# Kernel tuning notes

Measured on AMD Instinct MI355X. Metric: run time of the kernel, lower is better.

Reference implementation:

```python
import jax, jax.numpy as jnp
import numpy as np

MEM_DIM = 1024
N_CHILD = 16384

def _linear_params(key, out_dim, in_dim):
    kw, kb = jax.random.split(key)
    bound = 1.0 / np.sqrt(in_dim)
    W = jax.random.uniform(kw, (out_dim, in_dim), jnp.float32, -bound, bound)
    b = jax.random.uniform(kb, (out_dim,), jnp.float32, -bound, bound)
    return W, b

def setup_inputs() -> dict:
    key = jax.random.key(0)
    ks = jax.random.split(key, 7)
    child_c = jax.random.normal(ks[0], (N_CHILD, MEM_DIM), jnp.float32)
    child_h = jax.random.normal(ks[1], (N_CHILD, MEM_DIM), jnp.float32)
    child_h_sum = jax.random.normal(ks[2], (MEM_DIM,), jnp.float32)
    W_ih, b_ih = _linear_params(ks[3], MEM_DIM, MEM_DIM)
    W_fh, b_fh = _linear_params(ks[4], MEM_DIM, MEM_DIM)
    W_uh, b_uh = _linear_params(ks[5], MEM_DIM, MEM_DIM)
    W_oh, b_oh = _linear_params(ks[6], MEM_DIM, MEM_DIM)
    return {
        "child_c": child_c, "child_h": child_h, "child_h_sum": child_h_sum,
        "W_ih": W_ih, "b_ih": b_ih, "W_fh": W_fh, "b_fh": b_fh,
        "W_uh": W_uh, "b_uh": b_uh, "W_oh": W_oh, "b_oh": b_oh,
    }

def reference(child_c, child_h, child_h_sum,
              W_ih, b_ih, W_fh, b_fh, W_uh, b_uh, W_oh, b_oh):
    # Gate projections on the summed child hidden state: [mem_dim]
    i = jax.nn.sigmoid(child_h_sum @ W_ih.T + b_ih)
    o = jax.nn.sigmoid(child_h_sum @ W_oh.T + b_oh)
    u = jnp.tanh(child_h_sum @ W_uh.T + b_uh)
    # Per-child forget gates, batched (replaces the Python loop): [N, mem_dim]
    f = jax.nn.sigmoid(child_h @ W_fh.T + b_fh)
    fc = f * child_c                     # [N, mem_dim]
    c = i * u + jnp.sum(fc, axis=0)      # [mem_dim]
    h = o * jnp.tanh(c)                  # [mem_dim]
    return (c, h)
```

## Files before the change

kernel.cpp:

```cpp
#include <hip/hip_runtime.h>
#include <hip/hip_bf16.h>
#include <math.h>

#define MEM_DIM 1024
#define N_CHILD 16384

#define BM 128
#define BN 64
#define BK 64
#define KITERS (MEM_DIM / BK)

typedef __bf16 bf16_t;
typedef __bf16 bf16x4 __attribute__((ext_vector_type(4)));
typedef __bf16 bf16x8 __attribute__((ext_vector_type(8)));
typedef float f32x4 __attribute__((ext_vector_type(4)));

__device__ __forceinline__ void async_load16(const bf16_t* g, bf16_t* l) {
    __builtin_amdgcn_global_load_lds(
        (const __attribute__((address_space(1))) unsigned int*)g,
        (__attribute__((address_space(3))) unsigned int*)l,
        16, 0, 0);
}

__global__ __launch_bounds__(256) void cvt_bf16_kernel(const float* __restrict__ srcA, int n8A,
                                                       const float* __restrict__ srcB, int n8B,
                                                       bf16_t* __restrict__ dst) {
    int t = blockIdx.x * 256 + threadIdx.x;
    if (t < n8A + n8B) {
        const float* s = (t < n8A) ? (srcA + (size_t)t * 8)
                                   : (srcB + (size_t)(t - n8A) * 8);
        float4 a = *(const float4*)s;
        float4 b = *(const float4*)(s + 4);
        bf16x8 o = { (bf16_t)a.x, (bf16_t)a.y, (bf16_t)a.z, (bf16_t)a.w,
                     (bf16_t)b.x, (bf16_t)b.y, (bf16_t)b.z, (bf16_t)b.w };
        *(bf16x8*)(dst + (size_t)t * 8) = o;
    }
}

__global__ void gates_kernel(const float* __restrict__ hsum,
                             const float* __restrict__ W_ih, const float* __restrict__ b_ih,
                             const float* __restrict__ W_uh, const float* __restrict__ b_uh,
                             const float* __restrict__ W_oh, const float* __restrict__ b_oh,
                             float* __restrict__ acc_c, float* __restrict__ o_ws) {
    const int j = blockIdx.x;
    const int tid = threadIdx.x;
    const float* wi = W_ih + (size_t)j * MEM_DIM;
    const float* wu = W_uh + (size_t)j * MEM_DIM;
    const float* wo = W_oh + (size_t)j * MEM_DIM;
    float si = 0.f, su = 0.f, so = 0.f;
    for (int k = tid; k < MEM_DIM; k += 256) {
        float hv = hsum[k];
        si += wi[k] * hv;
        su += wu[k] * hv;
        so += wo[k] * hv;
    }
    for (int off = 32; off > 0; off >>= 1) {
        si += __shfl_down(si, off, 64);
        su += __shfl_down(su, off, 64);
        so += __shfl_down(so, off, 64);
    }
    __shared__ float red[3][4];
    const int wave = tid >> 6, lane = tid & 63;
    if (lane == 0) { red[0][wave] = si; red[1][wave] = su; red[2][wave] = so; }
    __syncthreads();
    if (tid == 0) {
        float ti = red[0][0] + red[0][1] + red[0][2] + red[0][3] + b_ih[j];
        float tu = red[1][0] + red[1][1] + red[1][2] + red[1][3] + b_uh[j];
        float to = red[2][0] + red[2][1] + red[2][2] + red[2][3] + b_oh[j];
        float iv = 1.f / (1.f + expf(-ti));
        float uv = tanhf(tu);
        float ov = 1.f / (1.f + expf(-to));
        acc_c[j] = iv * uv;
        o_ws[j]  = ov;
    }
}

__global__ __launch_bounds__(256, 4) void fused_gemm_bf16(
        const bf16_t* __restrict__ hbf, const bf16_t* __restrict__ wbf,
        const float* __restrict__ child_c, const float* __restrict__ b_fh,
        float* __restrict__ acc_c) {
    __shared__ __align__(1024) bf16_t sA[BM * BK];
    __shared__ __align__(1024) bf16_t sB[BN * BK];
    __shared__ float sred[BN];

    const int tid  = threadIdx.x;
    const int lane = tid & 63;
    const int wave = tid >> 6;
    const int wr = wave >> 1;
    const int wc = wave & 1;
    const int q  = lane >> 4;
    const int cl = lane & 15;

    const int b   = blockIdx.x;
    const int xcd = b & 7;
    const int l   = b >> 3;
    const int jt  = l & 15;
    const int ntl = l >> 4;
    const int j0  = jt * BN;
    const int n0  = (xcd * 16 + ntl) * BM;

    const int rl = lane >> 3;
    const int p  = lane & 7;
    const int cf = (p ^ rl) * 8;
    const bf16_t* gA[4];
    bf16_t* lA[4];
#pragma unroll
    for (int i = 0; i < 4; i++) {
        const int r = wave * 32 + i * 8 + rl;
        gA[i] = hbf + (size_t)(n0 + r) * MEM_DIM + cf;
        lA[i] = &sA[(wave * 32 + i * 8) * BK];
    }
    const bf16_t* gB[2];
    bf16_t* lB[2];
#pragma unroll
    for (int i = 0; i < 2; i++) {
        const int r = wave * 16 + i * 8 + rl;
        gB[i] = wbf + (size_t)(j0 + r) * MEM_DIM + cf;
        lB[i] = &sB[(wave * 16 + i * 8) * BK];
    }

    f32x4 acc[4][2];
#pragma unroll
    for (int a = 0; a < 4; a++)
#pragma unroll
        for (int c = 0; c < 2; c++) acc[a][c] = (f32x4)0.0f;

    for (int k = 0; k < KITERS; ++k) {
#pragma unroll
        for (int i = 0; i < 4; i++) { async_load16(gA[i], lA[i]); gA[i] += BK; }
#pragma unroll
        for (int i = 0; i < 2; i++) { async_load16(gB[i], lB[i]); gB[i] += BK; }
        __syncthreads();

#pragma unroll
        for (int h = 0; h < 2; h++) {
            bf16x8 af[4], bfr[2];
#pragma unroll
            for (int mt = 0; mt < 4; mt++) {
                const int ra = wr * 64 + mt * 16 + cl;
                af[mt] = *(const bf16x8*)(&sA[ra * BK + (((4 * h + q) ^ (cl & 7)) * 8)]);
            }
#pragma unroll
            for (int nt = 0; nt < 2; nt++) {
                const int rb = wc * 32 + nt * 16 + cl;
                bfr[nt] = *(const bf16x8*)(&sB[rb * BK + (((4 * h + q) ^ (cl & 7)) * 8)]);
            }
#pragma unroll
            for (int mt = 0; mt < 4; mt++)
#pragma unroll
                for (int nt = 0; nt < 2; nt++)
                    acc[mt][nt] = __builtin_amdgcn_mfma_f32_16x16x32_bf16(
                        af[mt], bfr[nt], acc[mt][nt], 0, 0, 0);
        }
        __syncthreads();
    }

    if (tid < BN) sred[tid] = 0.0f;
    __syncthreads();

    float colsum[2] = {0.f, 0.f};
#pragma unroll
    for (int nt = 0; nt < 2; nt++) {
        const int col = j0 + wc * 32 + nt * 16 + cl;
        const float bias = b_fh[col];
#pragma unroll
        for (int mt = 0; mt < 4; mt++) {
#pragma unroll
            for (int r = 0; r < 4; r++) {
                const int row = n0 + wr * 64 + mt * 16 + q * 4 + r;
                float s = acc[mt][nt][r] + bias;
                float fg = 1.0f / (1.0f + __expf(-s));
                colsum[nt] += fg * child_c[(size_t)row * MEM_DIM + col];
            }
        }
        colsum[nt] += __shfl_xor(colsum[nt], 16, 64);
        colsum[nt] += __shfl_xor(colsum[nt], 32, 64);
    }
    if (q == 0) {
#pragma unroll
        for (int nt = 0; nt < 2; nt++)
            atomicAdd(&sred[wc * 32 + nt * 16 + cl], colsum[nt]);
    }
    __syncthreads();
    if (tid < BN) atomicAdd(&acc_c[j0 + tid], sred[tid]);
}

#define LDS_STRIDE 40
__global__ __launch_bounds__(256) void fused_gemm_f32(
        const float* __restrict__ child_h, const float* __restrict__ child_c,
        const float* __restrict__ W_fh, const float* __restrict__ b_fh,
        float* __restrict__ acc_c) {
    __shared__ __align__(16) bf16_t sA[128 * LDS_STRIDE];
    __shared__ __align__(16) bf16_t sB[128 * LDS_STRIDE];
    __shared__ float sred[128];
    const int tid = threadIdx.x, lane = tid & 63, wave = tid >> 6;
    const int wr = wave >> 1, wc = wave & 1;
    const int j0 = blockIdx.x * 128, n0 = blockIdx.y * 128;
    const int q = lane >> 4, cl = lane & 15;
    f32x4 acc[4][4];
#pragma unroll
    for (int a = 0; a < 4; a++)
#pragma unroll
        for (int c = 0; c < 4; c++) acc[a][c] = (f32x4)0.0f;
    for (int k0 = 0; k0 < MEM_DIM; k0 += 32) {
#pragma unroll
        for (int i = 0; i < 4; i++) {
            int f = tid + i * 256, row = f >> 3, col = (f & 7) * 4;
            float4 va = *(const float4*)(child_h + (size_t)(n0 + row) * MEM_DIM + k0 + col);
            float4 vb = *(const float4*)(W_fh    + (size_t)(j0 + row) * MEM_DIM + k0 + col);
            bf16x4 ba = { (bf16_t)va.x, (bf16_t)va.y, (bf16_t)va.z, (bf16_t)va.w };
            bf16x4 bb = { (bf16_t)vb.x, (bf16_t)vb.y, (bf16_t)vb.z, (bf16_t)vb.w };
            *(bf16x4*)(&sA[row * LDS_STRIDE + col]) = ba;
            *(bf16x4*)(&sB[row * LDS_STRIDE + col]) = bb;
        }
        __syncthreads();
        bf16x8 af[4], bfr[4];
#pragma unroll
        for (int mt = 0; mt < 4; mt++) {
            af[mt]  = *(const bf16x8*)(&sA[(wr * 64 + mt * 16 + cl) * LDS_STRIDE + q * 8]);
            bfr[mt] = *(const bf16x8*)(&sB[(wc * 64 + mt * 16 + cl) * LDS_STRIDE + q * 8]);
        }
#pragma unroll
        for (int mt = 0; mt < 4; mt++)
#pragma unroll
            for (int nt = 0; nt < 4; nt++)
                acc[mt][nt] = __builtin_amdgcn_mfma_f32_16x16x32_bf16(af[mt], bfr[nt], acc[mt][nt], 0, 0, 0);
        __syncthreads();
    }
    if (tid < 128) sred[tid] = 0.0f;
    __syncthreads();
    float colsum[4] = {0.f, 0.f, 0.f, 0.f};
#pragma unroll
    for (int nt = 0; nt < 4; nt++) {
        const int col = j0 + wc * 64 + nt * 16 + cl;
        const float bias = b_fh[col];
#pragma unroll
        for (int mt = 0; mt < 4; mt++)
#pragma unroll
            for (int r = 0; r < 4; r++) {
                const int row = n0 + wr * 64 + mt * 16 + q * 4 + r;
                float s = acc[mt][nt][r] + bias;
                float fg = 1.0f / (1.0f + __expf(-s));
                colsum[nt] += fg * child_c[(size_t)row * MEM_DIM + col];
            }
        colsum[nt] += __shfl_xor(colsum[nt], 16, 64);
        colsum[nt] += __shfl_xor(colsum[nt], 32, 64);
    }
    if (q == 0)
#pragma unroll
        for (int nt = 0; nt < 4; nt++)
            atomicAdd(&sred[wc * 64 + nt * 16 + cl], colsum[nt]);
    __syncthreads();
    if (tid < 128) atomicAdd(&acc_c[j0 + tid], sred[tid]);
}

__global__ void finalize_kernel(const float* __restrict__ acc_c,
                                const float* __restrict__ o_ws,
                                float* __restrict__ out) {
    int t = blockIdx.x * 256 + threadIdx.x;
    if (t < MEM_DIM) {
        float cv = acc_c[t];
        float hv = o_ws[t] * tanhf(cv);
        out[t] = cv;
        out[MEM_DIM + t] = hv;
    }
}

extern "C" void kernel_launch(void* const* d_in, const int* in_sizes, int n_in,
                              void* d_out, int out_size, void* d_ws, size_t ws_size,
                              hipStream_t stream) {
    const float* child_c = (const float*)d_in[0];
    const float* child_h = (const float*)d_in[1];
    const float* hsum    = (const float*)d_in[2];
    const float* W_ih    = (const float*)d_in[3];
    const float* b_ih    = (const float*)d_in[4];
    const float* W_fh    = (const float*)d_in[5];
    const float* b_fh    = (const float*)d_in[6];
    const float* W_uh    = (const float*)d_in[7];
    const float* b_uh    = (const float*)d_in[8];
    const float* W_oh    = (const float*)d_in[9];
    const float* b_oh    = (const float*)d_in[10];
    float* out   = (float*)d_out;

    float* acc_c = (float*)d_ws;
    float* o_ws  = acc_c + MEM_DIM;
    const size_t HBF_OFF = 8192;
    const size_t HBF_BYTES = (size_t)N_CHILD * MEM_DIM * 2;
    const size_t WBF_BYTES = (size_t)MEM_DIM * MEM_DIM * 2;
    const size_t NEED = HBF_OFF + HBF_BYTES + WBF_BYTES;

    gates_kernel<<<MEM_DIM, 256, 0, stream>>>(hsum, W_ih, b_ih, W_uh, b_uh, W_oh, b_oh,
                                              acc_c, o_ws);

    if (ws_size >= NEED) {
        bf16_t* hbf = (bf16_t*)((char*)d_ws + HBF_OFF);
        bf16_t* wbf = hbf + (size_t)N_CHILD * MEM_DIM;
        int n8_h = (N_CHILD * MEM_DIM) / 8;
        int n8_w = (MEM_DIM * MEM_DIM) / 8;
        cvt_bf16_kernel<<<(n8_h + n8_w + 255) / 256, 256, 0, stream>>>(
            child_h, n8_h, W_fh, n8_w, hbf);
        fused_gemm_bf16<<<(N_CHILD / BM) * (MEM_DIM / BN), 256, 0, stream>>>(
            hbf, wbf, child_c, b_fh, acc_c);
    } else {
        dim3 grid(MEM_DIM / 128, N_CHILD / 128);
        fused_gemm_f32<<<grid, 256, 0, stream>>>(child_h, child_c, W_fh, b_fh, acc_c);
    }
    finalize_kernel<<<(MEM_DIM + 255) / 256, 256, 0, stream>>>(acc_c, o_ws, out);
}
```

Baseline: 214.0 us.

## Pre-tile bf16 operands into MFMA fragment layout and load directly to registers

The conversion kernel now writes child_h and W_fh in a tiled bf16 layout where each 16x32 block is stored in the exact per-lane order the 16x16x32 MFMA expects. The GEMM drops LDS staging, barriers and swizzled LDS reads. Each wave loads its fragments straight from global memory with 16-byte loads, double-buffered in registers. This removes LDS traffic and syncs but loses cross-wave sharing: each A/B fragment is now fetched by two waves from global/L2 instead of once into LDS.

```diff
diff --git a/kernel.cpp b/kernel.cpp
--- a/kernel.cpp
+++ b/kernel.cpp
@@ -7,34 +7,35 @@
 
 #define BM 128
 #define BN 64
-#define BK 64
-#define KITERS (MEM_DIM / BK)
 
 typedef __bf16 bf16_t;
-typedef __bf16 bf16x4 __attribute__((ext_vector_type(4)));
 typedef __bf16 bf16x8 __attribute__((ext_vector_type(8)));
 typedef float f32x4 __attribute__((ext_vector_type(4)));
 
-__device__ __forceinline__ void async_load16(const bf16_t* g, bf16_t* l) {
-    __builtin_amdgcn_global_load_lds(
-        (const __attribute__((address_space(1))) unsigned int*)g,
-        (__attribute__((address_space(3))) unsigned int*)l,
-        16, 0, 0);
-}
-
-__global__ __launch_bounds__(256) void cvt_bf16_kernel(const float* __restrict__ srcA, int n8A,
-                                                       const float* __restrict__ srcB, int n8B,
-                                                       bf16_t* __restrict__ dst) {
-    int t = blockIdx.x * 256 + threadIdx.x;
-    if (t < n8A + n8B) {
-        const float* s = (t < n8A) ? (srcA + (size_t)t * 8)
-                                   : (srcB + (size_t)(t - n8A) * 8);
-        float4 a = *(const float4*)s;
-        float4 b = *(const float4*)(s + 4);
-        bf16x8 o = { (bf16_t)a.x, (bf16_t)a.y, (bf16_t)a.z, (bf16_t)a.w,
-                     (bf16_t)b.x, (bf16_t)b.y, (bf16_t)b.z, (bf16_t)b.w };
-        *(bf16x8*)(dst + (size_t)t * 8) = o;
-    }
+
+__global__ __launch_bounds__(256) void cvt_tile_kernel(const float* __restrict__ srcA,
+                                                       int unitsA,
+                                                       const float* __restrict__ srcB,
+                                                       bf16_t* __restrict__ dst,
+                                                       int unitsTot) {
+    const int t = blockIdx.x * 256 + threadIdx.x;
+    const int unit = t >> 6;
+    if (unit >= unitsTot) return;
+    const int w  = (t & 63) * 8;
+    const int q  = w >> 7;
+    const int cl = (w >> 3) & 15;
+    const float* src;
+    int u;
+    if (unit < unitsA) { src = srcA; u = unit; }
+    else               { src = srcB; u = unit - unitsA; }
+    const int rb = u >> 5;
+    const int kt = u & 31;
+    src += (size_t)(rb * 16 + cl) * MEM_DIM + kt * 32 + q * 8;
+    float4 x = *(const float4*)src;
+    float4 y = *(const float4*)(src + 4);
+    bf16x8 o = { (bf16_t)x.x, (bf16_t)x.y, (bf16_t)x.z, (bf16_t)x.w,
+                 (bf16_t)y.x, (bf16_t)y.y, (bf16_t)y.z, (bf16_t)y.w };
+    *(bf16x8*)(dst + (size_t)t * 8) = o;
 }
 
 __global__ void gates_kernel(const float* __restrict__ hsum,
@@ -79,8 +80,6 @@
         const bf16_t* __restrict__ hbf, const bf16_t* __restrict__ wbf,
         const float* __restrict__ child_c, const float* __restrict__ b_fh,
         float* __restrict__ acc_c) {
-    __shared__ __align__(1024) bf16_t sA[BM * BK];
-    __shared__ __align__(1024) bf16_t sB[BN * BK];
     __shared__ float sred[BN];
 
     const int tid  = threadIdx.x;
@@ -99,25 +98,16 @@
     const int j0  = jt * BN;
     const int n0  = (xcd * 16 + ntl) * BM;
 
-    const int rl = lane >> 3;
-    const int p  = lane & 7;
-    const int cf = (p ^ rl) * 8;
-    const bf16_t* gA[4];
-    bf16_t* lA[4];
-#pragma unroll
-    for (int i = 0; i < 4; i++) {
-        const int r = wave * 32 + i * 8 + rl;
-        gA[i] = hbf + (size_t)(n0 + r) * MEM_DIM + cf;
-        lA[i] = &sA[(wave * 32 + i * 8) * BK];
-    }
-    const bf16_t* gB[2];
-    bf16_t* lB[2];
-#pragma unroll
-    for (int i = 0; i < 2; i++) {
-        const int r = wave * 16 + i * 8 + rl;
-        gB[i] = wbf + (size_t)(j0 + r) * MEM_DIM + cf;
-        lB[i] = &sB[(wave * 16 + i * 8) * BK];
-    }
+    const int nb0 = (n0 >> 4) + wr * 4;
+    const int jb0 = (j0 >> 4) + wc * 2;
+    const bf16_t* pA[4];
+    const bf16_t* pB[2];
+#pragma unroll
+    for (int mt = 0; mt < 4; mt++)
+        pA[mt] = hbf + ((size_t)(nb0 + mt) * 32) * 512 + lane * 8;
+#pragma unroll
+    for (int nt = 0; nt < 2; nt++)
+        pB[nt] = wbf + ((size_t)(jb0 + nt) * 32) * 512 + lane * 8;
 
     f32x4 acc[4][2];
 #pragma unroll
@@ -125,34 +115,30 @@
 #pragma unroll
         for (int c = 0; c < 2; c++) acc[a][c] = (f32x4)0.0f;
 
-    for (int k = 0; k < KITERS; ++k) {
-#pragma unroll
-        for (int i = 0; i < 4; i++) { async_load16(gA[i], lA[i]); gA[i] += BK; }
-#pragma unroll
-        for (int i = 0; i < 2; i++) { async_load16(gB[i], lB[i]); gB[i] += BK; }
-        __syncthreads();
-
-#pragma unroll
-        for (int h = 0; h < 2; h++) {
-            bf16x8 af[4], bfr[2];
-#pragma unroll
-            for (int mt = 0; mt < 4; mt++) {
-                const int ra = wr * 64 + mt * 16 + cl;
-                af[mt] = *(const bf16x8*)(&sA[ra * BK + (((4 * h + q) ^ (cl & 7)) * 8)]);
-            }
-#pragma unroll
-            for (int nt = 0; nt < 2; nt++) {
-                const int rb = wc * 32 + nt * 16 + cl;
-                bfr[nt] = *(const bf16x8*)(&sB[rb * BK + (((4 * h + q) ^ (cl & 7)) * 8)]);
-            }
-#pragma unroll
-            for (int mt = 0; mt < 4; mt++)
-#pragma unroll
-                for (int nt = 0; nt < 2; nt++)
-                    acc[mt][nt] = __builtin_amdgcn_mfma_f32_16x16x32_bf16(
-                        af[mt], bfr[nt], acc[mt][nt], 0, 0, 0);
-        }
-        __syncthreads();
+    bf16x8 af[2][4], bfr[2][2];
+
+    auto loadStage = [&](int s) {
+#pragma unroll
+        for (int mt = 0; mt < 4; mt++) { af[s][mt] = *(const bf16x8*)pA[mt]; pA[mt] += 512; }
+#pragma unroll
+        for (int nt = 0; nt < 2; nt++) { bfr[s][nt] = *(const bf16x8*)pB[nt]; pB[nt] += 512; }
+    };
+    auto compute = [&](int s) {
+#pragma unroll
+        for (int mt = 0; mt < 4; mt++)
+#pragma unroll
+            for (int nt = 0; nt < 2; nt++)
+                acc[mt][nt] = __builtin_amdgcn_mfma_f32_16x16x32_bf16(
+                    af[s][mt], bfr[s][nt], acc[mt][nt], 0, 0, 0);
+    };
+
+    loadStage(0);
+#pragma unroll 1
+    for (int it = 0; it < 16; ++it) {
+        loadStage(1);
+        compute(0);
+        if (it < 15) loadStage(0);
+        compute(1);
     }
 
     if (tid < BN) sred[tid] = 0.0f;
@@ -197,6 +183,7 @@
     const int wr = wave >> 1, wc = wave & 1;
     const int j0 = blockIdx.x * 128, n0 = blockIdx.y * 128;
     const int q = lane >> 4, cl = lane & 15;
+    typedef __bf16 bf16x4 __attribute__((ext_vector_type(4)));
     f32x4 acc[4][4];
 #pragma unroll
     for (int a = 0; a < 4; a++)
@@ -295,10 +282,12 @@
     if (ws_size >= NEED) {
         bf16_t* hbf = (bf16_t*)((char*)d_ws + HBF_OFF);
         bf16_t* wbf = hbf + (size_t)N_CHILD * MEM_DIM;
-        int n8_h = (N_CHILD * MEM_DIM) / 8;
-        int n8_w = (MEM_DIM * MEM_DIM) / 8;
-        cvt_bf16_kernel<<<(n8_h + n8_w + 255) / 256, 256, 0, stream>>>(
-            child_h, n8_h, W_fh, n8_w, hbf);
+        const int unitsA  = (N_CHILD / 16) * 32;
+        const int unitsB  = (MEM_DIM / 16) * 32;
+        const int unitsT  = unitsA + unitsB;
+        const int threads = unitsT * 64;
+        cvt_tile_kernel<<<(threads + 255) / 256, 256, 0, stream>>>(
+            child_h, unitsA, W_fh, hbf, unitsT);
         fused_gemm_bf16<<<(N_CHILD / BM) * (MEM_DIM / BN), 256, 0, stream>>>(
             hbf, wbf, child_c, b_fh, acc_c);
     } else {
```

New measurement: 231.6 us. 1.08x slower.
